# Performance work log

Measured on AMD Instinct MI355X. Metric: run time of the kernel, lower is better.

## Reference

```python
import jax, jax.numpy as jnp
import numpy as np
from jax import lax

DEPTH = 24
D_MODEL = 192
D_INNER = 384       # expand=2
D_STATE = 16
D_CONV = 4
DT_RANK = 12        # ceil(192/16)
NUM_CLASSES = 1000
PATCH = 16
IMG = 224
EPS = 1e-5


def setup_inputs() -> dict:
    key = jax.random.key(0)
    ks = jax.random.split(key, 20)
    s = 0.02
    inp = {
        "x": jax.random.normal(ks[0], (64, 3, IMG, IMG), dtype=jnp.float32),
        "patch_w": jax.random.normal(ks[1], (D_MODEL, 3, PATCH, PATCH), dtype=jnp.float32) * s,
        "patch_b": jnp.zeros((D_MODEL,), jnp.float32),
        "norm_w": jnp.ones((DEPTH, D_MODEL), jnp.float32),
        "norm_b": jnp.zeros((DEPTH, D_MODEL), jnp.float32),
        "in_proj_w": jax.random.normal(ks[2], (DEPTH, 2 * D_INNER, D_MODEL), dtype=jnp.float32) * s,
        "conv_w": jax.random.normal(ks[3], (DEPTH, D_INNER, D_CONV), dtype=jnp.float32) * 0.1,
        "conv_b": jnp.zeros((DEPTH, D_INNER), jnp.float32),
        "x_proj_w": jax.random.normal(ks[4], (DEPTH, DT_RANK + 2 * D_STATE, D_INNER), dtype=jnp.float32) * s,
        "dt_proj_w": jax.random.normal(ks[5], (DEPTH, D_INNER, DT_RANK), dtype=jnp.float32) * 0.1,
        "dt_proj_b": jax.random.normal(ks[6], (DEPTH, D_INNER), dtype=jnp.float32) * 0.1,
        "A_log": jnp.log(jnp.broadcast_to(jnp.arange(1, D_STATE + 1, dtype=jnp.float32), (DEPTH, D_INNER, D_STATE))),
        "D": jnp.ones((DEPTH, D_INNER), jnp.float32),
        "out_proj_w": jax.random.normal(ks[7], (DEPTH, D_MODEL, D_INNER), dtype=jnp.float32) * (s / np.sqrt(DEPTH)),
        "normf_w": jnp.ones((D_MODEL,), jnp.float32),
        "normf_b": jnp.zeros((D_MODEL,), jnp.float32),
        "head_w": jax.random.normal(ks[8], (NUM_CLASSES, D_MODEL), dtype=jnp.float32) * s,
        "head_b": jnp.zeros((NUM_CLASSES,), jnp.float32),
    }
    return inp


def _layernorm(h, w, b):
    mu = jnp.mean(h, axis=-1, keepdims=True)
    var = jnp.var(h, axis=-1, keepdims=True)
    return (h - mu) * lax.rsqrt(var + EPS) * w + b


def _mamba(h, in_w, cw, cb, xw, dtw, dtb, A_log, Dp, ow):
    # h: [B, L, D_MODEL]
    B, L, _ = h.shape
    xz = jnp.einsum('bld,ed->ble', h, in_w)            # [B,L,2*Di]
    x_in, z = xz[..., :D_INNER], xz[..., D_INNER:]
    # causal depthwise conv1d, kernel D_CONV
    xpad = jnp.pad(x_in, ((0, 0), (D_CONV - 1, 0), (0, 0)))
    xwin = jnp.stack([xpad[:, k:k + L, :] for k in range(D_CONV)], axis=-1)  # [B,L,Di,K]
    xc = jax.nn.silu(jnp.einsum('bldk,dk->bld', xwin, cw) + cb)
    # input-dependent dt, B, C
    dbc = jnp.einsum('bld,ed->ble', xc, xw)            # [B,L,DT_RANK+2N]
    dt = dbc[..., :DT_RANK]
    Bm = dbc[..., DT_RANK:DT_RANK + D_STATE]           # [B,L,N]
    Cm = dbc[..., DT_RANK + D_STATE:]                  # [B,L,N]
    delta = jax.nn.softplus(jnp.einsum('blr,dr->bld', dt, dtw) + dtb)  # [B,L,Di]
    A = -jnp.exp(A_log)                                # [Di,N]
    deltaA = jnp.exp(delta[..., None] * A)             # [B,L,Di,N]
    deltaBu = delta[..., None] * Bm[:, :, None, :] * xc[..., None]

    def step(hst, inp):
        dA, dBu, c = inp
        hst = dA * hst + dBu                           # [B,Di,N]
        y = jnp.einsum('bdn,bn->bd', hst, c)
        return hst, y

    h0 = jnp.zeros((B, D_INNER, D_STATE), deltaA.dtype)
    _, ys = lax.scan(step, h0, (deltaA.transpose(1, 0, 2, 3),
                                deltaBu.transpose(1, 0, 2, 3),
                                Cm.transpose(1, 0, 2)))
    y = ys.transpose(1, 0, 2) + Dp * xc                # [B,L,Di]
    y = y * jax.nn.silu(z)
    return jnp.einsum('ble,de->bld', y, ow)


def reference(x, patch_w, patch_b, norm_w, norm_b, in_proj_w, conv_w, conv_b,
              x_proj_w, dt_proj_w, dt_proj_b, A_log, D, out_proj_w,
              normf_w, normf_b, head_w, head_b):
    B = x.shape[0]
    G = IMG // PATCH  # 14
    xr = x.reshape(B, 3, G, PATCH, G, PATCH)
    tokens = jnp.einsum('bcipjq,ecpq->bije', xr, patch_w).reshape(B, G * G, D_MODEL) + patch_b
    residual = None
    hidden = tokens
    for i in range(DEPTH):
        residual = hidden if residual is None else residual + hidden
        hn = _layernorm(residual, norm_w[i], norm_b[i])
        hidden = _mamba(hn, in_proj_w[i], conv_w[i], conv_b[i], x_proj_w[i],
                        dt_proj_w[i], dt_proj_b[i], A_log[i], D[i], out_proj_w[i])
    # faithful: final branch sets residual = drop_path(hidden) (no add), then norms it
    hidden = _layernorm(hidden, normf_w, normf_b)
    feat = hidden[:, -1, :]                            # final_pool_type='none'
    return feat @ head_w.T + head_b
```

## Files before the change

kernel.cpp:

```cpp
#include <hip/hip_runtime.h>
#include <hip/hip_bf16.h>
#include <math.h>

#define DEPTH 24
#define D_MODEL 192
#define D_INNER 384
#define D_STATE 16
#define DT_RANK 12
#define NCLS 1000
#define PATCHSZ 16
#define IMG 224
#define GSZ 14
#define L_TOK 196
#define BATCH 64
#define M_ROWS (BATCH*L_TOK)
#define N_CH (BATCH*D_INNER)
#define EPSV 1e-5f
#define LOG2E 1.4426950408889634f

typedef __attribute__((ext_vector_type(8))) short bf16x8;
typedef __attribute__((ext_vector_type(4))) float f32x4;
typedef unsigned short ushort_t;
typedef unsigned int uint_t;

__device__ __forceinline__ float silu_(float x) { return x / (1.f + __expf(-x)); }

__device__ __forceinline__ ushort_t f2bf(float f) {
    uint_t u = __float_as_uint(f);
    u += 0x7fffu + ((u >> 16) & 1u);
    return (ushort_t)(u >> 16);
}
__device__ __forceinline__ float bf2f(ushort_t u) {
    return __uint_as_float(((uint_t)u) << 16);
}

__global__ __launch_bounds__(256) void f2bf_k(const float* __restrict__ s,
                                              ushort_t* __restrict__ d, int n) {
    for (int i = blockIdx.x * 256 + threadIdx.x; i < n; i += gridDim.x * 256)
        d[i] = f2bf(s[i]);
}

__global__ __launch_bounds__(256) void pad_xw_k(const float* __restrict__ s,
                                                ushort_t* __restrict__ d) {
    int idx = blockIdx.x * 256 + threadIdx.x;
    if (idx >= DEPTH * 64 * 384) return;
    int k = idx % 384, r = idx / 384;
    int n = r % 64, i = r / 64;
    d[idx] = (n < 44) ? f2bf(s[((size_t)i * 44 + n) * 384 + k]) : (ushort_t)0;
}

__global__ __launch_bounds__(256) void pad_dtw_k(const float* __restrict__ s,
                                                 ushort_t* __restrict__ d) {
    int idx = blockIdx.x * 256 + threadIdx.x;
    if (idx >= DEPTH * 384 * 32) return;
    int rr = idx % 32, q = idx / 32;
    int dd = q % 384, i = q / 384;
    d[idx] = (rr < 12) ? f2bf(s[((size_t)i * 384 + dd) * 12 + rr]) : (ushort_t)0;
}

__global__ __launch_bounds__(256) void im2col_k(const float* __restrict__ x,
                                                ushort_t* __restrict__ Acol) {
    int idx = blockIdx.x * 256 + threadIdx.x;
    if (idx >= M_ROWS * 768) return;
    int row = idx / 768, k = idx % 768;
    int b = row / L_TOK, l = row % L_TOK;
    int i = l / GSZ, j = l % GSZ;
    int c = k >> 8, r = k & 255, p = r >> 4, q = r & 15;
    Acol[idx] = f2bf(x[((size_t)(b * 3 + c) * IMG + (i * PATCHSZ + p)) * IMG + (j * PATCHSZ + q)]);
}

__global__ __launch_bounds__(256) void gemm_mfma(
    const ushort_t* __restrict__ A, int lda,
    const ushort_t* __restrict__ B, int ldb,
    float* __restrict__ C, int ldc,
    int N, int K, const float* __restrict__ bias, int act, int nvalid,
    ushort_t* __restrict__ dtpad, int mode,
    float2* __restrict__ dd2out, ushort_t* __restrict__ zbout,
    const ushort_t* __restrict__ xcbin)
{
    __shared__ uint4 AlsU[512];
    __shared__ uint4 BlsU[256];
    char* Als = (char*)AlsU;
    char* Bls = (char*)BlsU;
    const int t = threadIdx.x;
    const int wid = t >> 6, lane = t & 63;
    const int wm = wid >> 1, wn = wid & 1;
    const int l15 = lane & 15, l4 = lane >> 4;
    const int bm = blockIdx.y * 128, bn = blockIdx.x * 64;

    f32x4 acc[4][2];
#pragma unroll
    for (int i = 0; i < 4; ++i)
#pragma unroll
        for (int j = 0; j < 2; ++j) acc[i][j] = (f32x4){0.f, 0.f, 0.f, 0.f};

    const int arow = t >> 2, akb = t & 3;
    for (int k0 = 0; k0 < K; k0 += 32) {
#pragma unroll
        for (int it = 0; it < 2; ++it) {
            int c = t + it * 256;
            int row = c >> 2, kb = c & 3;
            uint4 v = *(const uint4*)(A + (size_t)(bm + row) * lda + k0 + kb * 8);
            *(uint4*)(Als + row * 64 + ((kb ^ (row & 3)) << 4)) = v;
        }
        {
            uint4 v = *(const uint4*)(B + (size_t)(bn + arow) * ldb + k0 + akb * 8);
            *(uint4*)(Bls + arow * 64 + ((akb ^ (arow & 3)) << 4)) = v;
        }
        __syncthreads();
        bf16x8 af[4], bfr[2];
#pragma unroll
        for (int fm = 0; fm < 4; ++fm) {
            int row = wm * 64 + fm * 16 + l15;
            af[fm] = *(const bf16x8*)(Als + row * 64 + ((l4 ^ (row & 3)) << 4));
        }
#pragma unroll
        for (int fn = 0; fn < 2; ++fn) {
            int row = wn * 32 + fn * 16 + l15;
            bfr[fn] = *(const bf16x8*)(Bls + row * 64 + ((l4 ^ (row & 3)) << 4));
        }
#pragma unroll
        for (int fm = 0; fm < 4; ++fm)
#pragma unroll
            for (int fn = 0; fn < 2; ++fn)
                acc[fm][fn] = __builtin_amdgcn_mfma_f32_16x16x32_bf16(af[fm], bfr[fn], acc[fm][fn], 0, 0, 0);
        __syncthreads();
    }

    if (mode == 2) {
#pragma unroll
        for (int fn = 0; fn < 2; ++fn) {
            int col = bn + wn * 32 + fn * 16 + l15;
            float bv = bias[col];
#pragma unroll
            for (int fm = 0; fm < 4; ++fm) {
                int row0 = bm + wm * 64 + fm * 16 + l4 * 4;
#pragma unroll
                for (int r = 0; r < 4; ++r) {
                    float v = acc[fm][fn][r] + bv;
                    v = (v > 20.f) ? v : log1pf(__expf(v));
                    float xv = bf2f(xcbin[(size_t)(row0 + r) * D_INNER + col]);
                    dd2out[(size_t)(row0 + r) * D_INNER + col] = make_float2(v, v * xv);
                }
            }
        }
    } else if (mode == 1) {
#pragma unroll
        for (int fn = 0; fn < 2; ++fn) {
            int col = bn + wn * 32 + fn * 16 + l15;
#pragma unroll
            for (int fm = 0; fm < 4; ++fm) {
                int row0 = bm + wm * 64 + fm * 16 + l4 * 4;
                if (col < D_INNER) {
#pragma unroll
                    for (int r = 0; r < 4; ++r)
                        C[(size_t)(row0 + r) * ldc + col] = acc[fm][fn][r];
                } else {
#pragma unroll
                    for (int r = 0; r < 4; ++r)
                        zbout[(size_t)(row0 + r) * D_INNER + (col - D_INNER)] = f2bf(acc[fm][fn][r]);
                }
            }
        }
    } else {
#pragma unroll
        for (int fn = 0; fn < 2; ++fn) {
            int col = bn + wn * 32 + fn * 16 + l15;
            float bv = (act >= 1 && bias) ? bias[col] : 0.f;
            bool cok = col < nvalid;
            bool dtc = dtpad && (col < 32);
#pragma unroll
            for (int fm = 0; fm < 4; ++fm) {
#pragma unroll
                for (int r = 0; r < 4; ++r) {
                    int row = bm + wm * 64 + fm * 16 + l4 * 4 + r;
                    float v = acc[fm][fn][r] + bv;
                    if (act == 2) v = (v > 20.f) ? v : log1pf(__expf(v));
                    if (cok) C[(size_t)row * ldc + col] = v;
                    if (dtc) dtpad[(size_t)row * 32 + col] = (col < 12) ? f2bf(v) : (ushort_t)0;
                }
            }
        }
    }
}

__global__ __launch_bounds__(256) void gemm_nt(
    const float* __restrict__ A, int lda,
    const float* __restrict__ B, int ldb,
    float* __restrict__ C, int ldc,
    int M, int N, int K,
    const float* __restrict__ bias, int act)
{
    __shared__ float As[16][68];
    __shared__ float Bs[16][68];
    const int t = threadIdx.x;
    const int tx = t & 15, ty = t >> 4;
    const int bm = blockIdx.y * 64, bn = blockIdx.x * 64;
    float acc[4][4] = {};
    const int kk = t & 15, m0 = t >> 4;

    for (int k0 = 0; k0 < K; k0 += 16) {
        int gk = k0 + kk;
        bool kok = gk < K;
#pragma unroll
        for (int p = 0; p < 4; ++p) {
            int mm = m0 + p * 16;
            int gm = bm + mm;
            As[kk][mm] = (kok && gm < M) ? A[(size_t)gm * lda + gk] : 0.f;
            int gn = bn + mm;
            Bs[kk][mm] = (kok && gn < N) ? B[(size_t)gn * ldb + gk] : 0.f;
        }
        __syncthreads();
#pragma unroll
        for (int k = 0; k < 16; ++k) {
            float4 av = *(const float4*)&As[k][ty * 4];
            float4 bv = *(const float4*)&Bs[k][tx * 4];
            acc[0][0] += av.x * bv.x; acc[0][1] += av.x * bv.y; acc[0][2] += av.x * bv.z; acc[0][3] += av.x * bv.w;
            acc[1][0] += av.y * bv.x; acc[1][1] += av.y * bv.y; acc[1][2] += av.y * bv.z; acc[1][3] += av.y * bv.w;
            acc[2][0] += av.z * bv.x; acc[2][1] += av.z * bv.y; acc[2][2] += av.z * bv.z; acc[2][3] += av.z * bv.w;
            acc[3][0] += av.w * bv.x; acc[3][1] += av.w * bv.y; acc[3][2] += av.w * bv.z; acc[3][3] += av.w * bv.w;
        }
        __syncthreads();
    }
#pragma unroll
    for (int i2 = 0; i2 < 4; ++i2) {
        int gm = bm + ty * 4 + i2;
        if (gm >= M) continue;
#pragma unroll
        for (int j = 0; j < 4; ++j) {
            int gn = bn + tx * 4 + j;
            if (gn >= N) continue;
            float v = acc[i2][j];
            if (act >= 1 && bias) v += bias[gn];
            C[(size_t)gm * ldc + gn] = v;
        }
    }
}

__global__ __launch_bounds__(256) void ln_resid_k(
    const float* __restrict__ hid, float* __restrict__ resid,
    ushort_t* __restrict__ hnb, const float* __restrict__ w,
    const float* __restrict__ b, int add)
{
    int wave = threadIdx.x >> 6, lane = threadIdx.x & 63;
    int row = blockIdx.x * 4 + wave;
    if (row >= M_ROWS) return;
    const float* hr = hid + (size_t)row * D_MODEL;
    float* rr = resid + (size_t)row * D_MODEL;
    float v[3];
#pragma unroll
    for (int j = 0; j < 3; ++j) {
        int e = lane + 64 * j;
        float h = hr[e];
        if (add) h += rr[e];
        rr[e] = h;
        v[j] = h;
    }
    float s = v[0] + v[1] + v[2];
    float sq = v[0] * v[0] + v[1] * v[1] + v[2] * v[2];
#pragma unroll
    for (int m = 1; m < 64; m <<= 1) {
        s += __shfl_xor(s, m, 64);
        sq += __shfl_xor(sq, m, 64);
    }
    float mu = s * (1.f / 192.f);
    float var = sq * (1.f / 192.f) - mu * mu;
    float ve = var + EPSV;
    float rs = rsqrtf(ve);
    rs = rs * (1.5f - 0.5f * ve * rs * rs);
    ushort_t* hnr = hnb + (size_t)row * D_MODEL;
#pragma unroll
    for (int j = 0; j < 3; ++j) {
        int e = lane + 64 * j;
        hnr[e] = f2bf((v[j] - mu) * rs * w[e] + b[e]);
    }
}

__global__ __launch_bounds__(256) void conv_silu_k(
    const float* __restrict__ xx, const float* __restrict__ cw,
    const float* __restrict__ cb, ushort_t* __restrict__ xcb)
{
    int idx = blockIdx.x * 256 + threadIdx.x;
    if (idx >= M_ROWS * D_INNER) return;
    int d = idx % D_INNER;
    int row = idx / D_INNER;
    int l = row % L_TOK;
    float acc = cb[d];
    const float* cwd = cw + d * 4;
#pragma unroll
    for (int k = 0; k < 4; ++k) {
        int ls = l + k - 3;
        if (ls >= 0) acc += xx[(size_t)(row + k - 3) * D_INNER + d] * cwd[k];
    }
    xcb[idx] = f2bf(silu_(acc));
}


__device__ __forceinline__ void dA_powers(float dl, float* dA) {
    float r1 = __expf(-dl);
    float r2 = r1 * r1, r3 = r2 * r1, r4 = r2 * r2;
    float r5 = r4 * r1, r6 = r4 * r2, r7 = r4 * r3, r8 = r4 * r4;
    dA[0] = r1;  dA[1] = r2;  dA[2] = r3;  dA[3] = r4;
    dA[4] = r5;  dA[5] = r6;  dA[6] = r7;  dA[7] = r8;
    dA[8] = r8 * r1;  dA[9] = r8 * r2;  dA[10] = r8 * r3;  dA[11] = r8 * r4;
    dA[12] = r8 * r5; dA[13] = r8 * r6; dA[14] = r8 * r7;  dA[15] = r8 * r8;
}

template<int CL>
__global__ __launch_bounds__(256) void scan_p1(
    const float2* __restrict__ dd2, const float* __restrict__ dbc,
    float* __restrict__ h_end, float* __restrict__ Ssum)
{
    int w = __builtin_amdgcn_readfirstlane(blockIdx.x * 4 + (threadIdx.x >> 6));
    int lane = threadIdx.x & 63;
    int dg = w % 6, b = (w / 6) % 64, c = w / 384;
    int d = dg * 64 + lane;
    int ch = b * D_INNER + d;

    size_t r0 = (size_t)b * L_TOK + (size_t)c * CL;
    const float2* pdd = dd2 + r0 * D_INNER + d;
    float2 dd[CL];
#pragma unroll
    for (int t = 0; t < CL; ++t) dd[t] = pdd[(size_t)t * D_INNER];

    float h[16];
#pragma unroll
    for (int n = 0; n < 16; ++n) h[n] = 0.f;
    float S = 0.f;
    const float4* pbq = (const float4*)(dbc + r0 * 44 + 12);
#pragma unroll
    for (int t = 0; t < CL; ++t) {
        float4 q0 = pbq[0], q1 = pbq[1], q2 = pbq[2], q3 = pbq[3];
        pbq += 11;
        float Bv[16] = {q0.x,q0.y,q0.z,q0.w, q1.x,q1.y,q1.z,q1.w,
                        q2.x,q2.y,q2.z,q2.w, q3.x,q3.y,q3.z,q3.w};
        float dl = dd[t].x, du = dd[t].y;
        S += dl;
        float dA[16];
        dA_powers(dl, dA);
#pragma unroll
        for (int n = 0; n < 16; ++n)
            h[n] = dA[n] * h[n] + du * Bv[n];
    }
#pragma unroll
    for (int n = 0; n < 16; ++n)
        h_end[((size_t)c * 16 + n) * N_CH + ch] = h[n];
    Ssum[(size_t)c * N_CH + ch] = S;
}

__global__ __launch_bounds__(256) void scan_p2(
    float* __restrict__ h_end, const float* __restrict__ Ssum, int nchunk)
{
    int idx = blockIdx.x * 256 + threadIdx.x;
    if (idx >= 16 * N_CH) return;
    int n = idx / N_CH, ch = idx % N_CH;
    float Av2 = -(float)(n + 1) * LOG2E;
    float H = 0.f;
    for (int c = 0; c < nchunk; ++c) {
        size_t o = (size_t)c * 16 * N_CH + idx;
        float e = h_end[o];
        float P = exp2f(Av2 * Ssum[(size_t)c * N_CH + ch]);
        float Hn = P * H + e;
        h_end[o] = H;
        H = Hn;
    }
}

template<int CL>
__global__ __launch_bounds__(256) void scan_p3(
    const float2* __restrict__ dd2, const ushort_t* __restrict__ xcb,
    const ushort_t* __restrict__ zb, const float* __restrict__ dbc,
    const float* __restrict__ Dp, const float* __restrict__ hstart,
    ushort_t* __restrict__ yb)
{
    int w = __builtin_amdgcn_readfirstlane(blockIdx.x * 4 + (threadIdx.x >> 6));
    int lane = threadIdx.x & 63;
    int dg = w % 6, b = (w / 6) % 64, c = w / 384;
    int d = dg * 64 + lane;
    int ch = b * D_INNER + d;
    float Dv = Dp[d];

    size_t r0 = (size_t)b * L_TOK + (size_t)c * CL;
    const float2* pdd = dd2 + r0 * D_INNER + d;
    const ushort_t* pxc = xcb + r0 * D_INNER + d;
    const ushort_t* pz = zb + r0 * D_INNER + d;
    float2 dd[CL]; ushort_t xv[CL]; ushort_t zv[CL];
#pragma unroll
    for (int t = 0; t < CL; ++t) dd[t] = pdd[(size_t)t * D_INNER];
#pragma unroll
    for (int t = 0; t < CL; ++t) xv[t] = pxc[(size_t)t * D_INNER];
#pragma unroll
    for (int t = 0; t < CL; ++t) zv[t] = pz[(size_t)t * D_INNER];

    float h[16];
#pragma unroll
    for (int n = 0; n < 16; ++n)
        h[n] = hstart[((size_t)c * 16 + n) * N_CH + ch];

    const float4* pbq = (const float4*)(dbc + r0 * 44 + 12);
    ushort_t* py = yb + r0 * D_INNER + d;
#pragma unroll
    for (int t = 0; t < CL; ++t) {
        float4 q0 = pbq[0], q1 = pbq[1], q2 = pbq[2], q3 = pbq[3];
        float4 q4 = pbq[4], q5 = pbq[5], q6 = pbq[6], q7 = pbq[7];
        pbq += 11;
        float Bv[16] = {q0.x,q0.y,q0.z,q0.w, q1.x,q1.y,q1.z,q1.w,
                        q2.x,q2.y,q2.z,q2.w, q3.x,q3.y,q3.z,q3.w};
        float Cv[16] = {q4.x,q4.y,q4.z,q4.w, q5.x,q5.y,q5.z,q5.w,
                        q6.x,q6.y,q6.z,q6.w, q7.x,q7.y,q7.z,q7.w};
        float dl = dd[t].x, du = dd[t].y;
        float dA[16];
        dA_powers(dl, dA);
        float y = 0.f;
#pragma unroll
        for (int n = 0; n < 16; ++n) {
            h[n] = dA[n] * h[n] + du * Bv[n];
            y += h[n] * Cv[n];
        }
        float xcf = bf2f(xv[t]);
        float zf = bf2f(zv[t]);
        py[(size_t)t * D_INNER] = f2bf((y + Dv * xcf) * silu_(zf));
    }
}

__global__ __launch_bounds__(64) void final_ln_k(
    const float* __restrict__ hid, const float* __restrict__ w,
    const float* __restrict__ b, float* __restrict__ feat)
{
    int bb = blockIdx.x;
    int lane = threadIdx.x;
    const float* hr = hid + ((size_t)bb * L_TOK + (L_TOK - 1)) * D_MODEL;
    float v[3];
#pragma unroll
    for (int j = 0; j < 3; ++j) v[j] = hr[lane + 64 * j];
    float s = v[0] + v[1] + v[2];
    float sq = v[0] * v[0] + v[1] * v[1] + v[2] * v[2];
#pragma unroll
    for (int m = 1; m < 64; m <<= 1) {
        s += __shfl_xor(s, m, 64);
        sq += __shfl_xor(sq, m, 64);
    }
    float mu = s * (1.f / 192.f);
    float var = sq * (1.f / 192.f) - mu * mu;
    float ve = var + EPSV;
    float rs = rsqrtf(ve);
    rs = rs * (1.5f - 0.5f * ve * rs * rs);
#pragma unroll
    for (int j = 0; j < 3; ++j) {
        int e = lane + 64 * j;
        feat[(size_t)bb * D_MODEL + e] = (v[j] - mu) * rs * w[e] + b[e];
    }
}

extern "C" void kernel_launch(void* const* d_in, const int* in_sizes, int n_in,
                              void* d_out, int out_size, void* d_ws, size_t ws_size,
                              hipStream_t stream) {
    const float* x         = (const float*)d_in[0];
    const float* patch_w   = (const float*)d_in[1];
    const float* patch_b   = (const float*)d_in[2];
    const float* norm_w    = (const float*)d_in[3];
    const float* norm_b    = (const float*)d_in[4];
    const float* in_proj_w = (const float*)d_in[5];
    const float* conv_w    = (const float*)d_in[6];
    const float* conv_b    = (const float*)d_in[7];
    const float* x_proj_w  = (const float*)d_in[8];
    const float* dt_proj_w = (const float*)d_in[9];
    const float* dt_proj_b = (const float*)d_in[10];
    const float* Dp        = (const float*)d_in[12];
    const float* out_proj_w= (const float*)d_in[13];
    const float* normf_w   = (const float*)d_in[14];
    const float* normf_b   = (const float*)d_in[15];
    const float* head_w    = (const float*)d_in[16];
    const float* head_b    = (const float*)d_in[17];
    float* out = (float*)d_out;

    float* ws = (float*)d_ws;
    size_t o = 0;
    float* resid = ws + o; o += (size_t)M_ROWS * D_MODEL;
    float* hid   = ws + o; o += (size_t)M_ROWS * D_MODEL;
    float* xx    = ws + o; o += (size_t)M_ROWS * D_INNER;
    ushort_t* zb = (ushort_t*)(ws + o); o += (size_t)M_ROWS * D_INNER / 2;
    float* dbc   = ws + o; o += (size_t)M_ROWS * 44;
    float2* dd2  = (float2*)(ws + o); o += (size_t)M_ROWS * D_INNER * 2;
    ushort_t* hnb = (ushort_t*)(ws + o); o += (size_t)M_ROWS * D_MODEL / 2;
    ushort_t* yb  = (ushort_t*)(ws + o); o += (size_t)M_ROWS * D_INNER / 2;
    ushort_t* xcb = (ushort_t*)(ws + o); o += (size_t)M_ROWS * D_INNER / 2;
    ushort_t* dtpadb = (ushort_t*)(ws + o); o += (size_t)M_ROWS * 32 / 2;
    ushort_t* iwb = (ushort_t*)(ws + o); o += (size_t)DEPTH * 768 * D_MODEL / 2;
    ushort_t* owb = (ushort_t*)(ws + o); o += (size_t)DEPTH * D_MODEL * D_INNER / 2;
    ushort_t* pwb = (ushort_t*)(ws + o); o += (size_t)D_MODEL * 768 / 2;
    ushort_t* xwb = (ushort_t*)(ws + o); o += (size_t)DEPTH * 64 * 384 / 2;
    ushort_t* dtwb = (ushort_t*)(ws + o); o += (size_t)DEPTH * 384 * 32 / 2;
    float* feat  = ws + o; o += (size_t)BATCH * D_MODEL;
    ushort_t* Acol = (ushort_t*)xx;

    int C = 14;
    if (o + (size_t)14 * 17 * N_CH > ws_size / 4) C = 7;
    float* h_end = ws + o;
    float* Ssum  = h_end + (size_t)C * 16 * N_CH;

    f2bf_k<<<2048, 256, 0, stream>>>(in_proj_w, iwb, DEPTH * 768 * D_MODEL);
    f2bf_k<<<2048, 256, 0, stream>>>(out_proj_w, owb, DEPTH * D_MODEL * D_INNER);
    f2bf_k<<<576, 256, 0, stream>>>(patch_w, pwb, D_MODEL * 768);
    pad_xw_k<<<(DEPTH * 64 * 384) / 256, 256, 0, stream>>>(x_proj_w, xwb);
    pad_dtw_k<<<(DEPTH * 384 * 32) / 256, 256, 0, stream>>>(dt_proj_w, dtwb);

    im2col_k<<<(M_ROWS * 768) / 256, 256, 0, stream>>>(x, Acol);
    {
        dim3 g(D_MODEL / 64, M_ROWS / 128);
        gemm_mfma<<<g, 256, 0, stream>>>(Acol, 768, pwb, 768, hid, D_MODEL,
                                         D_MODEL, 768, patch_b, 1, D_MODEL, nullptr,
                                         0, nullptr, nullptr, nullptr);
    }

    for (int i = 0; i < DEPTH; ++i) {
        const float* nw  = norm_w    + (size_t)i * D_MODEL;
        const float* nb  = norm_b    + (size_t)i * D_MODEL;
        const ushort_t* iw = iwb     + (size_t)i * 768 * D_MODEL;
        const float* cwp = conv_w    + (size_t)i * D_INNER * 4;
        const float* cbp = conv_b    + (size_t)i * D_INNER;
        const ushort_t* xwl = xwb    + (size_t)i * 64 * 384;
        const ushort_t* dtwl = dtwb  + (size_t)i * 384 * 32;
        const float* dtb = dt_proj_b + (size_t)i * D_INNER;
        const float* dp  = Dp        + (size_t)i * D_INNER;
        const ushort_t* ow = owb     + (size_t)i * D_MODEL * D_INNER;

        ln_resid_k<<<M_ROWS / 4, 256, 0, stream>>>(hid, resid, hnb, nw, nb, i > 0 ? 1 : 0);

        {
            dim3 g(768 / 64, M_ROWS / 128);
            gemm_mfma<<<g, 256, 0, stream>>>(hnb, D_MODEL, iw, D_MODEL, xx, D_INNER,
                                             768, D_MODEL, nullptr, 0, 768, nullptr,
                                             1, nullptr, zb, nullptr);
        }
        conv_silu_k<<<(M_ROWS * D_INNER) / 256, 256, 0, stream>>>(xx, cwp, cbp, xcb);
        {
            dim3 g(1, M_ROWS / 128);
            gemm_mfma<<<g, 256, 0, stream>>>(xcb, D_INNER, xwl, D_INNER, dbc, 44,
                                             64, D_INNER, nullptr, 0, 44, dtpadb,
                                             0, nullptr, nullptr, nullptr);
        }
        {
            dim3 g(D_INNER / 64, M_ROWS / 128);
            gemm_mfma<<<g, 256, 0, stream>>>(dtpadb, 32, dtwl, 32, nullptr, 0,
                                             D_INNER, 32, dtb, 2, D_INNER, nullptr,
                                             2, dd2, nullptr, xcb);
        }
        if (C == 14) {
            scan_p1<14><<<96 * 14, 256, 0, stream>>>(dd2, dbc, h_end, Ssum);
            scan_p2<<<(16 * N_CH) / 256, 256, 0, stream>>>(h_end, Ssum, 14);
            scan_p3<14><<<96 * 14, 256, 0, stream>>>(dd2, xcb, zb, dbc, dp, h_end, yb);
        } else {
            scan_p1<28><<<96 * 7, 256, 0, stream>>>(dd2, dbc, h_end, Ssum);
            scan_p2<<<(16 * N_CH) / 256, 256, 0, stream>>>(h_end, Ssum, 7);
            scan_p3<28><<<96 * 7, 256, 0, stream>>>(dd2, xcb, zb, dbc, dp, h_end, yb);
        }
        {
            dim3 g(D_MODEL / 64, M_ROWS / 128);
            gemm_mfma<<<g, 256, 0, stream>>>(yb, D_INNER, ow, D_INNER, hid, D_MODEL,
                                             D_MODEL, D_INNER, nullptr, 0, D_MODEL, nullptr,
                                             0, nullptr, nullptr, nullptr);
        }
    }

    final_ln_k<<<BATCH, 64, 0, stream>>>(hid, normf_w, normf_b, feat);
    {
        dim3 g((NCLS + 63) / 64, (BATCH + 63) / 64);
        gemm_nt<<<g, 256, 0, stream>>>(feat, D_MODEL, head_w, D_MODEL, out, NCLS,
                                       BATCH, NCLS, D_MODEL, head_b, 1);
    }
}
```

Baseline: 3.556 ms.

## Store xx in bf16, drop packed delta*x buffer, use finer scan chunks

The in_proj GEMM now writes the x half in bf16, and conv reads bf16, which halves that intermediate's traffic. The dt_proj GEMM writes only fp32 delta; the scan kernels load xcb and compute delta*x themselves instead of reading a float2 buffer. The scan is split into 28 chunks of 7 tokens, falling back to 14, to raise parallelism. The cost is more h_end/Ssum storage and traffic plus slightly lower precision for the conv input.

```diff
diff --git a/kernel.cpp b/kernel.cpp
--- a/kernel.cpp
+++ b/kernel.cpp
@@ -74,9 +74,7 @@
     const ushort_t* __restrict__ B, int ldb,
     float* __restrict__ C, int ldc,
     int N, int K, const float* __restrict__ bias, int act, int nvalid,
-    ushort_t* __restrict__ dtpad, int mode,
-    float2* __restrict__ dd2out, ushort_t* __restrict__ zbout,
-    const ushort_t* __restrict__ xcbin)
+    ushort_t* __restrict__ sout, int mode, ushort_t* __restrict__ zbout)
 {
     __shared__ uint4 AlsU[512];
     __shared__ uint4 BlsU[256];
@@ -127,24 +125,7 @@
         __syncthreads();
     }
 
-    if (mode == 2) {
-#pragma unroll
-        for (int fn = 0; fn < 2; ++fn) {
-            int col = bn + wn * 32 + fn * 16 + l15;
-            float bv = bias[col];
-#pragma unroll
-            for (int fm = 0; fm < 4; ++fm) {
-                int row0 = bm + wm * 64 + fm * 16 + l4 * 4;
-#pragma unroll
-                for (int r = 0; r < 4; ++r) {
-                    float v = acc[fm][fn][r] + bv;
-                    v = (v > 20.f) ? v : log1pf(__expf(v));
-                    float xv = bf2f(xcbin[(size_t)(row0 + r) * D_INNER + col]);
-                    dd2out[(size_t)(row0 + r) * D_INNER + col] = make_float2(v, v * xv);
-                }
-            }
-        }
-    } else if (mode == 1) {
+    if (mode == 1) {
 #pragma unroll
         for (int fn = 0; fn < 2; ++fn) {
             int col = bn + wn * 32 + fn * 16 + l15;
@@ -154,7 +135,7 @@
                 if (col < D_INNER) {
 #pragma unroll
                     for (int r = 0; r < 4; ++r)
-                        C[(size_t)(row0 + r) * ldc + col] = acc[fm][fn][r];
+                        sout[(size_t)(row0 + r) * D_INNER + col] = f2bf(acc[fm][fn][r]);
                 } else {
 #pragma unroll
                     for (int r = 0; r < 4; ++r)
@@ -168,7 +149,7 @@
             int col = bn + wn * 32 + fn * 16 + l15;
             float bv = (act >= 1 && bias) ? bias[col] : 0.f;
             bool cok = col < nvalid;
-            bool dtc = dtpad && (col < 32);
+            bool dtc = sout && (col < 32);
 #pragma unroll
             for (int fm = 0; fm < 4; ++fm) {
 #pragma unroll
@@ -177,7 +158,7 @@
                     float v = acc[fm][fn][r] + bv;
                     if (act == 2) v = (v > 20.f) ? v : log1pf(__expf(v));
                     if (cok) C[(size_t)row * ldc + col] = v;
-                    if (dtc) dtpad[(size_t)row * 32 + col] = (col < 12) ? f2bf(v) : (ushort_t)0;
+                    if (dtc) sout[(size_t)row * 32 + col] = (col < 12) ? f2bf(v) : (ushort_t)0;
                 }
             }
         }
@@ -277,7 +258,7 @@
 }
 
 __global__ __launch_bounds__(256) void conv_silu_k(
-    const float* __restrict__ xx, const float* __restrict__ cw,
+    const ushort_t* __restrict__ xxb, const float* __restrict__ cw,
     const float* __restrict__ cb, ushort_t* __restrict__ xcb)
 {
     int idx = blockIdx.x * 256 + threadIdx.x;
@@ -290,7 +271,7 @@
 #pragma unroll
     for (int k = 0; k < 4; ++k) {
         int ls = l + k - 3;
-        if (ls >= 0) acc += xx[(size_t)(row + k - 3) * D_INNER + d] * cwd[k];
+        if (ls >= 0) acc += bf2f(xxb[(size_t)(row + k - 3) * D_INNER + d]) * cwd[k];
     }
     xcb[idx] = f2bf(silu_(acc));
 }
@@ -308,8 +289,9 @@
 
 template<int CL>
 __global__ __launch_bounds__(256) void scan_p1(
-    const float2* __restrict__ dd2, const float* __restrict__ dbc,
-    float* __restrict__ h_end, float* __restrict__ Ssum)
+    const float* __restrict__ delta, const ushort_t* __restrict__ xcb,
+    const float* __restrict__ dbc, float* __restrict__ h_end,
+    float* __restrict__ Ssum)
 {
     int w = __builtin_amdgcn_readfirstlane(blockIdx.x * 4 + (threadIdx.x >> 6));
     int lane = threadIdx.x & 63;
@@ -318,10 +300,13 @@
     int ch = b * D_INNER + d;
 
     size_t r0 = (size_t)b * L_TOK + (size_t)c * CL;
-    const float2* pdd = dd2 + r0 * D_INNER + d;
-    float2 dd[CL];
-#pragma unroll
-    for (int t = 0; t < CL; ++t) dd[t] = pdd[(size_t)t * D_INNER];
+    const float* pd = delta + r0 * D_INNER + d;
+    const ushort_t* pxc = xcb + r0 * D_INNER + d;
+    float dl[CL]; ushort_t xv[CL];
+#pragma unroll
+    for (int t = 0; t < CL; ++t) dl[t] = pd[(size_t)t * D_INNER];
+#pragma unroll
+    for (int t = 0; t < CL; ++t) xv[t] = pxc[(size_t)t * D_INNER];
 
     float h[16];
 #pragma unroll
@@ -334,10 +319,11 @@
         pbq += 11;
         float Bv[16] = {q0.x,q0.y,q0.z,q0.w, q1.x,q1.y,q1.z,q1.w,
                         q2.x,q2.y,q2.z,q2.w, q3.x,q3.y,q3.z,q3.w};
-        float dl = dd[t].x, du = dd[t].y;
-        S += dl;
+        float d_ = dl[t];
+        float du = d_ * bf2f(xv[t]);
+        S += d_;
         float dA[16];
-        dA_powers(dl, dA);
+        dA_powers(d_, dA);
 #pragma unroll
         for (int n = 0; n < 16; ++n)
             h[n] = dA[n] * h[n] + du * Bv[n];
@@ -368,7 +354,7 @@
 
 template<int CL>
 __global__ __launch_bounds__(256) void scan_p3(
-    const float2* __restrict__ dd2, const ushort_t* __restrict__ xcb,
+    const float* __restrict__ delta, const ushort_t* __restrict__ xcb,
     const ushort_t* __restrict__ zb, const float* __restrict__ dbc,
     const float* __restrict__ Dp, const float* __restrict__ hstart,
     ushort_t* __restrict__ yb)
@@ -381,12 +367,12 @@
     float Dv = Dp[d];
 
     size_t r0 = (size_t)b * L_TOK + (size_t)c * CL;
-    const float2* pdd = dd2 + r0 * D_INNER + d;
+    const float* pd = delta + r0 * D_INNER + d;
     const ushort_t* pxc = xcb + r0 * D_INNER + d;
     const ushort_t* pz = zb + r0 * D_INNER + d;
-    float2 dd[CL]; ushort_t xv[CL]; ushort_t zv[CL];
-#pragma unroll
-    for (int t = 0; t < CL; ++t) dd[t] = pdd[(size_t)t * D_INNER];
+    float dl[CL]; ushort_t xv[CL]; ushort_t zv[CL];
+#pragma unroll
+    for (int t = 0; t < CL; ++t) dl[t] = pd[(size_t)t * D_INNER];
 #pragma unroll
     for (int t = 0; t < CL; ++t) xv[t] = pxc[(size_t)t * D_INNER];
 #pragma unroll
@@ -408,16 +394,17 @@
                         q2.x,q2.y,q2.z,q2.w, q3.x,q3.y,q3.z,q3.w};
         float Cv[16] = {q4.x,q4.y,q4.z,q4.w, q5.x,q5.y,q5.z,q5.w,
                         q6.x,q6.y,q6.z,q6.w, q7.x,q7.y,q7.z,q7.w};
-        float dl = dd[t].x, du = dd[t].y;
+        float d_ = dl[t];
+        float xcf = bf2f(xv[t]);
+        float du = d_ * xcf;
         float dA[16];
-        dA_powers(dl, dA);
+        dA_powers(d_, dA);
         float y = 0.f;
 #pragma unroll
         for (int n = 0; n < 16; ++n) {
             h[n] = dA[n] * h[n] + du * Bv[n];
             y += h[n] * Cv[n];
         }
-        float xcf = bf2f(xv[t]);
         float zf = bf2f(zv[t]);
         py[(size_t)t * D_INNER] = f2bf((y + Dv * xcf) * silu_(zf));
     }
@@ -478,10 +465,10 @@
     size_t o = 0;
     float* resid = ws + o; o += (size_t)M_ROWS * D_MODEL;
     float* hid   = ws + o; o += (size_t)M_ROWS * D_MODEL;
-    float* xx    = ws + o; o += (size_t)M_ROWS * D_INNER;
-    ushort_t* zb = (ushort_t*)(ws + o); o += (size_t)M_ROWS * D_INNER / 2;
+    ushort_t* xxb = (ushort_t*)(ws + o); o += (size_t)M_ROWS * D_INNER / 2;
+    ushort_t* zb  = (ushort_t*)(ws + o); o += (size_t)M_ROWS * D_INNER / 2;
     float* dbc   = ws + o; o += (size_t)M_ROWS * 44;
-    float2* dd2  = (float2*)(ws + o); o += (size_t)M_ROWS * D_INNER * 2;
+    float* delta = ws + o; o += (size_t)M_ROWS * D_INNER;
     ushort_t* hnb = (ushort_t*)(ws + o); o += (size_t)M_ROWS * D_MODEL / 2;
     ushort_t* yb  = (ushort_t*)(ws + o); o += (size_t)M_ROWS * D_INNER / 2;
     ushort_t* xcb = (ushort_t*)(ws + o); o += (size_t)M_ROWS * D_INNER / 2;
@@ -492,10 +479,10 @@
     ushort_t* xwb = (ushort_t*)(ws + o); o += (size_t)DEPTH * 64 * 384 / 2;
     ushort_t* dtwb = (ushort_t*)(ws + o); o += (size_t)DEPTH * 384 * 32 / 2;
     float* feat  = ws + o; o += (size_t)BATCH * D_MODEL;
-    ushort_t* Acol = (ushort_t*)xx;
-
-    int C = 14;
-    if (o + (size_t)14 * 17 * N_CH > ws_size / 4) C = 7;
+    ushort_t* Acol = (ushort_t*)delta;
+
+    int C = 28;
+    if (o + (size_t)28 * 17 * N_CH > ws_size / 4) C = 14;
     float* h_end = ws + o;
     float* Ssum  = h_end + (size_t)C * 16 * N_CH;
 
@@ -509,8 +496,8 @@
     {
         dim3 g(D_MODEL / 64, M_ROWS / 128);
         gemm_mfma<<<g, 256, 0, stream>>>(Acol, 768, pwb, 768, hid, D_MODEL,
-                                         D_MODEL, 768, patch_b, 1, D_MODEL, nullptr,
-                                         0, nullptr, nullptr, nullptr);
+                                         D_MODEL, 768, patch_b, 1, D_MODEL,
+                                         nullptr, 0, nullptr);
     }
 
     for (int i = 0; i < DEPTH; ++i) {
@@ -529,37 +516,37 @@
 
         {
             dim3 g(768 / 64, M_ROWS / 128);
-            gemm_mfma<<<g, 256, 0, stream>>>(hnb, D_MODEL, iw, D_MODEL, xx, D_INNER,
-                                             768, D_MODEL, nullptr, 0, 768, nullptr,
-                                             1, nullptr, zb, nullptr);
-        }
-        conv_silu_k<<<(M_ROWS * D_INNER) / 256, 256, 0, stream>>>(xx, cwp, cbp, xcb);
+            gemm_mfma<<<g, 256, 0, stream>>>(hnb, D_MODEL, iw, D_MODEL, nullptr, 0,
+                                             768, D_MODEL, nullptr, 0, 768,
+                                             xxb, 1, zb);
+        }
+        conv_silu_k<<<(M_ROWS * D_INNER) / 256, 256, 0, stream>>>(xxb, cwp, cbp, xcb);
         {
             dim3 g(1, M_ROWS / 128);
             gemm_mfma<<<g, 256, 0, stream>>>(xcb, D_INNER, xwl, D_INNER, dbc, 44,
-                                             64, D_INNER, nullptr, 0, 44, dtpadb,
-                                             0, nullptr, nullptr, nullptr);
+                                             64, D_INNER, nullptr, 0, 44,
+                                             dtpadb, 0, nullptr);
         }
         {
             dim3 g(D_INNER / 64, M_ROWS / 128);
-            gemm_mfma<<<g, 256, 0, stream>>>(dtpadb, 32, dtwl, 32, nullptr, 0,
-                                             D_INNER, 32, dtb, 2, D_INNER, nullptr,
-                                             2, dd2, nullptr, xcb);
-        }
-        if (C == 14) {
-            scan_p1<14><<<96 * 14, 256, 0, stream>>>(dd2, dbc, h_end, Ssum);
+            gemm_mfma<<<g, 256, 0, stream>>>(dtpadb, 32, dtwl, 32, delta, D_INNER,
+                                             D_INNER, 32, dtb, 2, D_INNER,
+                                             nullptr, 0, nullptr);
+        }
+        if (C == 28) {
+            scan_p1<7><<<96 * 28, 256, 0, stream>>>(delta, xcb, dbc, h_end, Ssum);
+            scan_p2<<<(16 * N_CH) / 256, 256, 0, stream>>>(h_end, Ssum, 28);
+            scan_p3<7><<<96 * 28, 256, 0, stream>>>(delta, xcb, zb, dbc, dp, h_end, yb);
+        } else {
+            scan_p1<14><<<96 * 14, 256, 0, stream>>>(delta, xcb, dbc, h_end, Ssum);
             scan_p2<<<(16 * N_CH) / 256, 256, 0, stream>>>(h_end, Ssum, 14);
-            scan_p3<14><<<96 * 14, 256, 0, stream>>>(dd2, xcb, zb, dbc, dp, h_end, yb);
-        } else {
-            scan_p1<28><<<96 * 7, 256, 0, stream>>>(dd2, dbc, h_end, Ssum);
-            scan_p2<<<(16 * N_CH) / 256, 256, 0, stream>>>(h_end, Ssum, 7);
-            scan_p3<28><<<96 * 7, 256, 0, stream>>>(dd2, xcb, zb, dbc, dp, h_end, yb);
+            scan_p3<14><<<96 * 14, 256, 0, stream>>>(delta, xcb, zb, dbc, dp, h_end, yb);
         }
         {
             dim3 g(D_MODEL / 64, M_ROWS / 128);
             gemm_mfma<<<g, 256, 0, stream>>>(yb, D_INNER, ow, D_INNER, hid, D_MODEL,
-                                             D_MODEL, D_INNER, nullptr, 0, D_MODEL, nullptr,
-                                             0, nullptr, nullptr, nullptr);
+                                             D_MODEL, D_INNER, nullptr, 0, D_MODEL,
+                                             nullptr, 0, nullptr);
         }
     }
 
```

New measurement: 3.622 ms. Within noise of the previous version (+1.8%).
